# Kernel optimization log

Measured on AMD Instinct MI355X. Metric: run time of the kernel, lower is better.

The kernel has to match this reference:

```python
import jax, jax.numpy as jnp
import numpy as np

B, F_IN, D_IN = 1024, 64, 64
N_CAPS, D_CAPS = 32, 64
ROUTINGS = 3
HEADS = 2
EPS = 1e-7  # K.epsilon()


def setup_inputs() -> dict:
    key = jax.random.key(0)
    ks = jax.random.split(key, 8)
    P = N_CAPS * (N_CAPS - 1) // 2
    return {
        "x": jax.random.normal(ks[0], (B, F_IN, D_IN), jnp.float32),
        "reweight_W": jax.random.normal(ks[1], (D_IN, N_CAPS, D_CAPS), jnp.float32) * 0.05,
        "routing_init": 10.0 * jax.random.truncated_normal(ks[2], -2.0, 2.0, (N_CAPS, F_IN), jnp.float32),
        "kernel_fm": jnp.full((N_CAPS, 1), 0.5, jnp.float32),
        "bias_fm": jnp.zeros((D_CAPS,), jnp.float32),
        "kernel_mf": jnp.ones((P, 1), jnp.float32),
        "bias_mf": jnp.zeros((D_CAPS,), jnp.float32),
        "kernel_highint": jnp.full((N_CAPS, 1), 0.5, jnp.float32),
        "bias_highint": jnp.zeros((D_CAPS * HEADS,), jnp.float32),
        "W_query": jax.random.normal(ks[3], (D_CAPS, D_CAPS * HEADS), jnp.float32) * 0.05,
        "W_key": jax.random.normal(ks[4], (D_CAPS, D_CAPS * HEADS), jnp.float32) * 0.05,
        "W_value": jax.random.normal(ks[5], (D_CAPS, D_CAPS * HEADS), jnp.float32) * 0.05,
        "W_res": jax.random.normal(ks[6], (D_CAPS, D_CAPS * HEADS), jnp.float32) * 0.05,
    }


def _squash(v):
    s = jnp.sum(v * v, axis=-1, keepdims=True) + EPS
    return (jnp.sqrt(s) / (0.5 + s)) * v


def _heads(t):
    # [B,N,H*F] -> [H,B,N,F] (matches tf.stack(tf.split(t, H, axis=2)))
    b, n, _ = t.shape
    return t.reshape(b, n, HEADS, D_CAPS).transpose(2, 0, 1, 3)


def reference(x, reweight_W, routing_init, kernel_fm, bias_fm, kernel_mf, bias_mf,
              kernel_highint, bias_highint, W_query, W_key, W_value, W_res):
    # inputs_hat: [B, N, F, C]
    inputs_hat = jnp.einsum('bfd,dnc->bnfc', x, reweight_W)
    b_logits = jnp.broadcast_to(routing_init[None], (x.shape[0], N_CAPS, F_IN))
    for _ in range(ROUTINGS):
        c = jax.nn.softmax(b_logits, axis=1)            # softmax over capsules
        outputs = _squash(jnp.einsum('bnf,bnfc->bnc', c, inputs_hat))
        b_logits = b_logits + jnp.einsum('bnc,bnfc->bnf', outputs, inputs_hat)
    c = jax.nn.softmax(b_logits, axis=1)
    routing_score = c[..., None]                        # [B,N,F,1]
    attention_output = routing_score * inputs_hat       # [B,N,F,C]

    # FM per-field: square-of-sum minus sum-of-square over input capsules
    sum_f = jnp.sum(attention_output, axis=2)           # [B,N,C]
    field_fm = sum_f ** 2 - jnp.sum(attention_output ** 2, axis=2)
    hi_fm = jnp.sum(field_fm * kernel_fm[None], axis=1) + bias_fm  # [B,C]

    field_wise_vectors = sum_f                          # [B,N,C]

    # pairwise MF interactions (itertools.combinations order == triu indices)
    li, ri = np.triu_indices(N_CAPS, k=1)
    emb_prod = field_wise_vectors[:, li] * field_wise_vectors[:, ri]  # [B,P,C]
    h_mf = jnp.sum(emb_prod * kernel_mf[None], axis=1) + bias_mf      # [B,C]

    # InteractingLayer (multi-head self-attention over fields, use_res=True)
    q = _heads(jnp.einsum('bnd,de->bne', field_wise_vectors, W_query))  # [H,B,N,F]
    k = _heads(jnp.einsum('bnd,de->bne', field_wise_vectors, W_key))
    v = _heads(jnp.einsum('bnd,de->bne', field_wise_vectors, W_value))
    attn = jax.nn.softmax(jnp.einsum('hbnf,hbmf->hbnm', q, k), axis=-1)
    out = jnp.einsum('hbnm,hbmf->hbnf', attn, v)        # [H,B,N,F]
    out = out.transpose(1, 2, 0, 3).reshape(x.shape[0], N_CAPS, HEADS * D_CAPS)
    res = jnp.einsum('bnd,de->bne', field_wise_vectors, W_res)
    fv2 = jax.nn.relu(out + res)                        # [B,N,H*F]
    high_int = jnp.sum(fv2 * kernel_highint[None], axis=1) + bias_highint  # [B,2C]

    return jnp.concatenate([hi_fm, h_mf, high_int], axis=-1), routing_score
```

## Files before the change

kernel.cpp:

```cpp
#include <hip/hip_runtime.h>


#define EPS_SQ 1e-7f

typedef __attribute__((ext_vector_type(8))) short bf16x8;
typedef __attribute__((ext_vector_type(4))) float floatx4;

__device__ __forceinline__ int lidx(int r, int c) {
  return r * 68 + ((((c >> 2) ^ (r >> 2)) & 15) << 2) + (c & 3);
}
__device__ __forceinline__ unsigned short f2bf(float f) {
  unsigned u = __float_as_uint(f);
  u += 0x7FFFu + ((u >> 16) & 1u);
  return (unsigned short)(u >> 16);
}

__global__ __launch_bounds__(256) void k_upd(
    const float* __restrict__ x, const float* __restrict__ rinit,
    const float* __restrict__ ow, float* __restrict__ blog,
    float* __restrict__ xc, float* __restrict__ rs, int iter)
{
  __shared__ __align__(16) float xs[64 * 68];
  __shared__ __align__(16) float owS[32 * 68];
  __shared__ __align__(16) float bS[32 * 68];
  const int b = blockIdx.x, t = threadIdx.x;
  const float* xb = x + b * 4096;

#pragma unroll
  for (int k = 0; k < 4; k++) {
    int lin = t + 256 * k; int f = lin >> 4; int d0 = (lin & 15) << 2;
    *(float4*)&xs[lidx(f, d0)] = *(const float4*)(xb + f * 64 + d0);
  }
  {
    const float* src = (iter <= 1) ? rinit : (blog + b * 2048);
#pragma unroll
    for (int k = 0; k < 2; k++) {
      int lin = t + 256 * k; int n = lin >> 4; int f0 = (lin & 15) << 2;
      *(float4*)&bS[lidx(n, f0)] = *(const float4*)(src + n * 64 + f0);
    }
  }
  if (iter > 0) {
#pragma unroll
    for (int k = 0; k < 2; k++) {
      int lin = t + 256 * k; int n = lin >> 4; int d0 = (lin & 15) << 2;
      *(float4*)&owS[lidx(n, d0)] = *(const float4*)(ow + b * 2048 + n * 64 + d0);
    }
  }
  __syncthreads();

  const int tn = t >> 4, tlo = t & 15;

  if (iter > 0) {
    const int n0 = tn * 2, f0 = tlo * 4;
    float acc[2][4] = {{0, 0, 0, 0}, {0, 0, 0, 0}};
    for (int dq = 0; dq < 64; dq += 4) {
      float o[2][4];
      *(float4*)o[0] = *(const float4*)&owS[lidx(n0, dq)];
      *(float4*)o[1] = *(const float4*)&owS[lidx(n0 + 1, dq)];
#pragma unroll
      for (int i = 0; i < 4; i++) {
        float xr[4];
        *(float4*)xr = *(const float4*)&xs[lidx(f0 + i, dq)];
#pragma unroll
        for (int k = 0; k < 4; k++) {
          acc[0][i] += o[0][k] * xr[k];
          acc[1][i] += o[1][k] * xr[k];
        }
      }
    }
#pragma unroll
    for (int j = 0; j < 2; j++) {
      float tmp[4];
      *(float4*)tmp = *(const float4*)&bS[lidx(n0 + j, f0)];
#pragma unroll
      for (int i = 0; i < 4; i++) tmp[i] += acc[j][i];
      *(float4*)&bS[lidx(n0 + j, f0)] = *(float4*)tmp;
    }
    __syncthreads();
    if (iter < 3) {
#pragma unroll
      for (int k = 0; k < 2; k++) {
        int lin = t + 256 * k; int n = lin >> 4; int f0b = (lin & 15) << 2;
        *(float4*)(blog + b * 2048 + n * 64 + f0b) = *(const float4*)&bS[lidx(n, f0b)];
      }
    }
    __syncthreads();
  }

  {
    const int n = t & 31, fg = t >> 5;
#pragma unroll
    for (int k = 0; k < 8; k++) {
      int f = fg * 8 + k;
      float v = bS[lidx(n, f)];
      float m = v;
      for (int s = 16; s > 0; s >>= 1) m = fmaxf(m, __shfl_xor(m, s, 64));
      float e = __expf(v - m);
      float sum = e;
      for (int s = 16; s > 0; s >>= 1) sum += __shfl_xor(sum, s, 64);
      bS[lidx(n, f)] = e / sum;
    }
  }
  __syncthreads();

  if (iter == 3) {
#pragma unroll
    for (int k = 0; k < 8; k++) {
      int lin = t + 256 * k; int n = lin >> 6, f = lin & 63;
      rs[b * 2048 + n * 64 + f] = bS[lidx(n, f)];
    }
  }
  {
    const int n0 = tn * 2, d0 = tlo * 4;
    float acc[2][4] = {{0, 0, 0, 0}, {0, 0, 0, 0}};
    for (int f = 0; f < 64; f++) {
      float c0v = bS[lidx(n0, f)];
      float c1v = bS[lidx(n0 + 1, f)];
      float xr[4];
      *(float4*)xr = *(const float4*)&xs[lidx(f, d0)];
#pragma unroll
      for (int i = 0; i < 4; i++) {
        acc[0][i] += c0v * xr[i];
        acc[1][i] += c1v * xr[i];
      }
    }
#pragma unroll
    for (int j = 0; j < 2; j++)
      *(float4*)(xc + b * 2048 + (n0 + j) * 64 + d0) = *(float4*)acc[j];
  }
}

__global__ __launch_bounds__(256) void k_sow(
    const float* __restrict__ W, const float* __restrict__ xc,
    float* __restrict__ ow)
{
  __shared__ __align__(16) float Mn[64 * 68];
  __shared__ __align__(16) float xcS[32 * 68];
  __shared__ __align__(16) float sS[32 * 68];
  __shared__ float scaleS[32];
  const int n = blockIdx.x & 31, b0 = (blockIdx.x >> 5) * 32, t = threadIdx.x;

#pragma unroll
  for (int k = 0; k < 4; k++) {
    int lin = t + 256 * k; int d = lin >> 4; int c0 = (lin & 15) << 2;
    *(float4*)&Mn[lidx(d, c0)] = *(const float4*)(W + d * 2048 + n * 64 + c0);
  }
#pragma unroll
  for (int k = 0; k < 2; k++) {
    int lin = t + 256 * k; int bb = lin >> 4; int d0 = (lin & 15) << 2;
    *(float4*)&xcS[lidx(bb, d0)] = *(const float4*)(xc + (b0 + bb) * 2048 + n * 64 + d0);
  }
  __syncthreads();

  const int bb0 = (t >> 4) * 2, c4 = (t & 15) * 4;
  {
    float acc[2][4] = {};
    for (int dq = 0; dq < 64; dq += 4) {
      float xv0[4], xv1[4];
      *(float4*)xv0 = *(const float4*)&xcS[lidx(bb0, dq)];
      *(float4*)xv1 = *(const float4*)&xcS[lidx(bb0 + 1, dq)];
#pragma unroll
      for (int j = 0; j < 4; j++) {
        float mr[4];
        *(float4*)mr = *(const float4*)&Mn[lidx(dq + j, c4)];
#pragma unroll
        for (int c = 0; c < 4; c++) {
          acc[0][c] += xv0[j] * mr[c];
          acc[1][c] += xv1[j] * mr[c];
        }
      }
    }
    *(float4*)&sS[lidx(bb0, c4)] = *(float4*)acc[0];
    *(float4*)&sS[lidx(bb0 + 1, c4)] = *(float4*)acc[1];
  }
  __syncthreads();
  if (t < 32) {
    float ss = EPS_SQ;
    for (int c = 0; c < 64; c++) { float v = sS[lidx(t, c)]; ss += v * v; }
    scaleS[t] = sqrtf(ss) / (0.5f + ss);
  }
  __syncthreads();
  {
    float a2[2][4] = {};
    for (int cq = 0; cq < 64; cq += 4) {
      float sv0[4], sv1[4];
      *(float4*)sv0 = *(const float4*)&sS[lidx(bb0, cq)];
      *(float4*)sv1 = *(const float4*)&sS[lidx(bb0 + 1, cq)];
#pragma unroll
      for (int j = 0; j < 4; j++) {
        float mr[4];
        *(float4*)mr = *(const float4*)&Mn[lidx(c4 + j, cq)];
        float s0 = 0.f, s1 = 0.f;
#pragma unroll
        for (int k = 0; k < 4; k++) { s0 += sv0[k] * mr[k]; s1 += sv1[k] * mr[k]; }
        a2[0][j] += s0; a2[1][j] += s1;
      }
    }
#pragma unroll
    for (int i = 0; i < 2; i++) {
      float sc = scaleS[bb0 + i];
      float outv[4];
#pragma unroll
      for (int j = 0; j < 4; j++) outv[j] = a2[i][j] * sc;
      *(float4*)(ow + (b0 + bb0 + i) * 2048 + n * 64 + c4) = *(float4*)outv;
    }
  }
}

__global__ __launch_bounds__(256) void k_fwv(
    const float* __restrict__ W, const float* __restrict__ xc,
    float* __restrict__ fwv)
{
  __shared__ __align__(16) float Mn[64 * 68];
  __shared__ __align__(16) float xcS[32 * 68];
  const int n = blockIdx.x & 31, b0 = (blockIdx.x >> 5) * 32, t = threadIdx.x;

#pragma unroll
  for (int k = 0; k < 4; k++) {
    int lin = t + 256 * k; int d = lin >> 4; int c0 = (lin & 15) << 2;
    *(float4*)&Mn[lidx(d, c0)] = *(const float4*)(W + d * 2048 + n * 64 + c0);
  }
#pragma unroll
  for (int k = 0; k < 2; k++) {
    int lin = t + 256 * k; int bb = lin >> 4; int d0 = (lin & 15) << 2;
    *(float4*)&xcS[lidx(bb, d0)] = *(const float4*)(xc + (b0 + bb) * 2048 + n * 64 + d0);
  }
  __syncthreads();

  const int bb0 = (t >> 4) * 2, c4 = (t & 15) * 4;
  float acc[2][4] = {};
  for (int dq = 0; dq < 64; dq += 4) {
    float xv0[4], xv1[4];
    *(float4*)xv0 = *(const float4*)&xcS[lidx(bb0, dq)];
    *(float4*)xv1 = *(const float4*)&xcS[lidx(bb0 + 1, dq)];
#pragma unroll
    for (int j = 0; j < 4; j++) {
      float mr[4];
      *(float4*)mr = *(const float4*)&Mn[lidx(dq + j, c4)];
#pragma unroll
      for (int c = 0; c < 4; c++) {
        acc[0][c] += xv0[j] * mr[c];
        acc[1][c] += xv1[j] * mr[c];
      }
    }
  }
  *(float4*)(fwv + (b0 + bb0) * 2048 + n * 64 + c4) = *(float4*)acc[0];
  *(float4*)(fwv + (b0 + bb0 + 1) * 2048 + n * 64 + c4) = *(float4*)acc[1];
}

__global__ __launch_bounds__(256) void k_ih(
    const float* __restrict__ x, const float* __restrict__ W,
    const float* __restrict__ rs, float* __restrict__ ssq)
{
  __shared__ __align__(16) unsigned short xB[4 * 64 * 64];
  __shared__ __align__(16) unsigned short wB[2 * 64 * 64];
  __shared__ float cF2[4 * 2 * 64];
  const int n0 = (blockIdx.x & 15) * 2, g = blockIdx.x >> 4;
  const int b0 = g * 4;
  const int t = threadIdx.x, w = t >> 6, lane = t & 63;

#pragma unroll
  for (int k = 0; k < 16; k++) {
    int ch = t + 256 * k;
    int bb = ch >> 10, rem = ch & 1023;
    int f = rem >> 4, fq = rem & 15;
    int dg = fq >> 1, half = fq & 1;
    float4 v = *(const float4*)(x + ((b0 + bb) * 64 + f) * 64 + fq * 4);
    unsigned int p0 = f2bf(v.x) | ((unsigned)f2bf(v.y) << 16);
    unsigned int p1 = f2bf(v.z) | ((unsigned)f2bf(v.w) << 16);
    *(uint2*)&xB[bb * 4096 + f * 64 + ((dg ^ (f & 7)) << 3) + half * 4] =
        make_uint2(p0, p1);
  }
  {
    int dd = t >> 2, cq = t & 3;
    int dg = dd >> 3, dl = dd & 7;
#pragma unroll
    for (int nn = 0; nn < 2; nn++) {
      const float* wp = W + dd * 2048 + (n0 + nn) * 64 + cq * 16;
      unsigned short* base = wB + nn * 4096;
#pragma unroll
      for (int i4 = 0; i4 < 4; i4++) {
        float4 v = *(const float4*)(wp + i4 * 4);
        float vv[4] = {v.x, v.y, v.z, v.w};
#pragma unroll
        for (int j = 0; j < 4; j++) {
          int c = cq * 16 + i4 * 4 + j;
          base[c * 64 + ((dg ^ (c & 7)) << 3) + dl] = f2bf(vv[j]);
        }
      }
    }
  }
  {
#pragma unroll
    for (int nn = 0; nn < 2; nn++) {
      float v = rs[(b0 + w) * 2048 + (n0 + nn) * 64 + lane];
      cF2[(w * 2 + nn) * 64 + lane] = v * v;
    }
  }
  __syncthreads();

  const int m = lane & 15, q = lane >> 4, ms = m & 7;

  bf16x8 a[4][2];
#pragma unroll
  for (int mi = 0; mi < 4; mi++) {
    const unsigned short* bp = xB + w * 4096 + (mi * 16 + m) * 64;
#pragma unroll
    for (int kk = 0; kk < 2; kk++)
      a[mi][kk] = *(const bf16x8*)&bp[((kk * 4 + q) ^ ms) << 3];
  }

#pragma unroll
  for (int nn = 0; nn < 2; nn++) {
    bf16x8 bf[4][2];
#pragma unroll
    for (int ci = 0; ci < 4; ci++) {
      const unsigned short* bp = wB + nn * 4096 + (ci * 16 + m) * 64;
#pragma unroll
      for (int kk = 0; kk < 2; kk++)
        bf[ci][kk] = *(const bf16x8*)&bp[((kk * 4 + q) ^ ms) << 3];
    }
    float ps[4] = {0.f, 0.f, 0.f, 0.f};
    const float* cf = cF2 + (w * 2 + nn) * 64 + q * 4;
#pragma unroll
    for (int mi = 0; mi < 4; mi++) {
      float cfv[4];
#pragma unroll
      for (int r = 0; r < 4; r++) cfv[r] = cf[mi * 16 + r];
#pragma unroll
      for (int ci = 0; ci < 4; ci++) {
        floatx4 c0 = {0.f, 0.f, 0.f, 0.f};
        c0 = __builtin_amdgcn_mfma_f32_16x16x32_bf16(a[mi][0], bf[ci][0], c0, 0, 0, 0);
        c0 = __builtin_amdgcn_mfma_f32_16x16x32_bf16(a[mi][1], bf[ci][1], c0, 0, 0, 0);
#pragma unroll
        for (int r = 0; r < 4; r++) { float tv = c0[r]; ps[ci] += cfv[r] * tv * tv; }
      }
    }
#pragma unroll
    for (int ci = 0; ci < 4; ci++) {
      ps[ci] += __shfl_xor(ps[ci], 16, 64);
      ps[ci] += __shfl_xor(ps[ci], 32, 64);
    }
    if (q == 0) {
#pragma unroll
      for (int ci = 0; ci < 4; ci++)
        ssq[(b0 + w) * 2048 + (n0 + nn) * 64 + ci * 16 + m] = ps[ci];
    }
  }
}

__global__ __launch_bounds__(256) void k_prep(
    const float* __restrict__ Wq, const float* __restrict__ Wk,
    const float* __restrict__ kmf, float* __restrict__ Ab, float* __restrict__ Kb)
{
  const int t = threadIdx.x;
  if (blockIdx.x < 8) {
    __shared__ __align__(16) float wkS[64 * 68];
    __shared__ __align__(16) float wqS[16 * 68];
    const int h = blockIdx.x & 1, rg = blockIdx.x >> 1;
#pragma unroll
    for (int k = 0; k < 4; k++) {
      int lin = t + 256 * k; int dp = lin >> 4; int e0 = (lin & 15) << 2;
      *(float4*)&wkS[lidx(dp, e0)] = *(const float4*)(Wk + dp * 128 + h * 64 + e0);
    }
    {
      int dl = t >> 4, e0 = (t & 15) << 2;
      *(float4*)&wqS[lidx(dl, e0)] = *(const float4*)(Wq + (rg * 16 + dl) * 128 + h * 64 + e0);
    }
    __syncthreads();
    const int dl = t >> 4, dp0 = (t & 15) << 2;
    float acc[4] = {};
    for (int e = 0; e < 64; e += 4) {
      float q4[4];
      *(float4*)q4 = *(const float4*)&wqS[lidx(dl, e)];
#pragma unroll
      for (int c = 0; c < 4; c++) {
        float mr[4];
        *(float4*)mr = *(const float4*)&wkS[lidx(dp0 + c, e)];
        acc[c] += q4[0] * mr[0] + q4[1] * mr[1] + q4[2] * mr[2] + q4[3] * mr[3];
      }
    }
    *(float4*)(Ab + h * 4096 + (rg * 16 + dl) * 64 + dp0) = *(float4*)acc;
  } else {
    __shared__ float Ks[1024];
    *(float4*)&Ks[t * 4] = make_float4(0.f, 0.f, 0.f, 0.f);
    __syncthreads();
    if (t < 248) {
#pragma unroll
      for (int j = 0; j < 2; j++) {
        int p = t * 2 + j;
        if (p < 496) {
          int l = 0, rem = p;
          while (rem >= 31 - l) { rem -= 31 - l; ++l; }
          int r = l + 1 + rem;
          float v = kmf[p];
          Ks[l * 32 + r] = v;
          Ks[r * 32 + l] = v;
        }
      }
    }
    __syncthreads();
    *(float4*)&Kb[t * 4] = *(const float4*)&Ks[t * 4];
  }
}

__global__ __launch_bounds__(256) void k_attn(
    const float* __restrict__ fwv, const float* __restrict__ ssq,
    const float* __restrict__ Ab, const float* __restrict__ Kb,
    const float* __restrict__ Wv, const float* __restrict__ Wr,
    const float* __restrict__ kfm, const float* __restrict__ bfm,
    const float* __restrict__ bmf, const float* __restrict__ khi,
    const float* __restrict__ bhi, float* __restrict__ out0)
{
  __shared__ __align__(16) float smem[8640];
  float* fwS  = smem;
  float* pS   = smem + 2176;
  float* bufA = smem + 4288;
  float* tS   = smem + 6464;
  float* vS   = smem + 4288;
  float* redH = smem + 2176;
  float* Kf   = smem + 4288;
  float* red1 = smem + 5312;

  const int b = blockIdx.x, t = threadIdx.x;
  const int tn = t >> 4, te = t & 15;
  const int n0 = tn * 2, e0 = te * 8, d0 = te * 4;

#pragma unroll
  for (int k = 0; k < 2; k++) {
    int lin = t + 256 * k; int nn = lin >> 4; int c0 = (lin & 15) << 2;
    *(float4*)&fwS[lidx(nn, c0)] = *(const float4*)(fwv + b * 2048 + nn * 64 + c0);
  }
  __syncthreads();

  for (int h = 0; h < 2; h++) {
    float tacc[2][4] = {};
    for (int half = 0; half < 2; half++) {
#pragma unroll
      for (int k = 0; k < 2; k++) {
        int lin = t + 256 * k; int d = lin >> 4; int c0 = (lin & 15) << 2;
        *(float4*)&bufA[lidx(d, c0)] =
            *(const float4*)(Ab + h * 4096 + (half * 32 + d) * 64 + c0);
      }
      __syncthreads();
      for (int dq = 0; dq < 32; dq += 4) {
        float fw0[4], fw1[4];
        *(float4*)fw0 = *(const float4*)&fwS[lidx(n0, half * 32 + dq)];
        *(float4*)fw1 = *(const float4*)&fwS[lidx(n0 + 1, half * 32 + dq)];
#pragma unroll
        for (int j = 0; j < 4; j++) {
          float mr[4];
          *(float4*)mr = *(const float4*)&bufA[lidx(dq + j, d0)];
#pragma unroll
          for (int c = 0; c < 4; c++) {
            tacc[0][c] += fw0[j] * mr[c];
            tacc[1][c] += fw1[j] * mr[c];
          }
        }
      }
      __syncthreads();
    }
    *(float4*)&tS[lidx(n0, d0)] = *(float4*)tacc[0];
    *(float4*)&tS[lidx(n0 + 1, d0)] = *(float4*)tacc[1];
    __syncthreads();
    {
      const int m0 = te * 2;
      float s00 = 0.f, s01 = 0.f, s10 = 0.f, s11 = 0.f;
      for (int kk = 0; kk < 16; kk++) {
        float ta0[4], ta1[4], f0[4], f1[4];
        *(float4*)ta0 = *(const float4*)&tS[lidx(n0, kk * 4)];
        *(float4*)ta1 = *(const float4*)&tS[lidx(n0 + 1, kk * 4)];
        *(float4*)f0 = *(const float4*)&fwS[lidx(m0, kk * 4)];
        *(float4*)f1 = *(const float4*)&fwS[lidx(m0 + 1, kk * 4)];
#pragma unroll
        for (int j = 0; j < 4; j++) {
          s00 += ta0[j] * f0[j]; s01 += ta0[j] * f1[j];
          s10 += ta1[j] * f0[j]; s11 += ta1[j] * f1[j];
        }
      }
      pS[(h * 32 + n0) * 33 + m0] = s00;
      pS[(h * 32 + n0) * 33 + m0 + 1] = s01;
      pS[(h * 32 + n0 + 1) * 33 + m0] = s10;
      pS[(h * 32 + n0 + 1) * 33 + m0 + 1] = s11;
    }
    __syncthreads();
  }

  if (t < 64) {
    const int base = t * 33;
    float mx = -1e30f;
    for (int m = 0; m < 32; m++) mx = fmaxf(mx, pS[base + m]);
    float sum = 0.f;
    for (int m = 0; m < 32; m++) { float e = __expf(pS[base + m] - mx); pS[base + m] = e; sum += e; }
    float inv = 1.0f / sum;
    for (int m = 0; m < 32; m++) pS[base + m] *= inv;
  }
  __syncthreads();

  {
    float acc[2][8] = {};
    for (int dq = 0; dq < 64; dq += 4) {
      float fw0[4], fw1[4];
      *(float4*)fw0 = *(const float4*)&fwS[lidx(n0, dq)];
      *(float4*)fw1 = *(const float4*)&fwS[lidx(n0 + 1, dq)];
#pragma unroll
      for (int jj = 0; jj < 4; jj++) {
        float w8[8];
        *(float4*)&w8[0] = *(const float4*)(Wv + (dq + jj) * 128 + e0);
        *(float4*)&w8[4] = *(const float4*)(Wv + (dq + jj) * 128 + e0 + 4);
#pragma unroll
        for (int j = 0; j < 8; j++) {
          acc[0][j] += fw0[jj] * w8[j];
          acc[1][j] += fw1[jj] * w8[j];
        }
      }
    }
    *(float4*)&vS[n0 * 132 + e0] = *(float4*)&acc[0][0];
    *(float4*)&vS[n0 * 132 + e0 + 4] = *(float4*)&acc[0][4];
    *(float4*)&vS[(n0 + 1) * 132 + e0] = *(float4*)&acc[1][0];
    *(float4*)&vS[(n0 + 1) * 132 + e0 + 4] = *(float4*)&acc[1][4];
  }
  __syncthreads();

  {
    const int h2 = te >> 3;
    float pacc[2][8] = {};
    for (int m = 0; m < 32; m++) {
      float p0 = pS[(h2 * 32 + n0) * 33 + m];
      float p1 = pS[(h2 * 32 + n0 + 1) * 33 + m];
      float vr[8];
      *(float4*)&vr[0] = *(const float4*)&vS[m * 132 + e0];
      *(float4*)&vr[4] = *(const float4*)&vS[m * 132 + e0 + 4];
#pragma unroll
      for (int j = 0; j < 8; j++) {
        pacc[0][j] += p0 * vr[j];
        pacc[1][j] += p1 * vr[j];
      }
    }
    for (int dq = 0; dq < 64; dq += 4) {
      float fw0[4], fw1[4];
      *(float4*)fw0 = *(const float4*)&fwS[lidx(n0, dq)];
      *(float4*)fw1 = *(const float4*)&fwS[lidx(n0 + 1, dq)];
#pragma unroll
      for (int jj = 0; jj < 4; jj++) {
        float w8[8];
        *(float4*)&w8[0] = *(const float4*)(Wr + (dq + jj) * 128 + e0);
        *(float4*)&w8[4] = *(const float4*)(Wr + (dq + jj) * 128 + e0 + 4);
#pragma unroll
        for (int j = 0; j < 8; j++) {
          pacc[0][j] += fw0[jj] * w8[j];
          pacc[1][j] += fw1[jj] * w8[j];
        }
      }
    }
    __syncthreads();
    {
      float kh0 = khi[n0], kh1 = khi[n0 + 1];
      float ph[8];
#pragma unroll
      for (int j = 0; j < 8; j++)
        ph[j] = kh0 * fmaxf(pacc[0][j], 0.f) + kh1 * fmaxf(pacc[1][j], 0.f);
      *(float4*)&redH[tn * 132 + e0] = *(float4*)&ph[0];
      *(float4*)&redH[tn * 132 + e0 + 4] = *(float4*)&ph[4];
    }
  }
  *(float4*)&Kf[t * 4] = *(const float4*)(Kb + t * 4);
  __syncthreads();

  if (t < 128) {
    float s = 0.f;
#pragma unroll
    for (int k = 0; k < 16; k++) s += redH[k * 132 + t];
    out0[b * 256 + 128 + t] = s + bhi[t];
  }
  {
    const int c = t & 63, nq = t >> 6;
    float p = 0.f;
#pragma unroll
    for (int k = 0; k < 8; k++) {
      int nn = nq * 8 + k;
      float fv = fwS[lidx(nn, c)];
      float sv = ssq[b * 2048 + nn * 64 + c];
      p += (fv * fv - sv) * kfm[nn];
    }
    red1[nq * 68 + c] = p;
    float inner[8] = {};
    for (int r = 0; r < 32; r++) {
      float fr = fwS[lidx(r, c)];
#pragma unroll
      for (int l8 = 0; l8 < 8; l8++)
        inner[l8] += Kf[(nq * 8 + l8) * 32 + r] * fr;
    }
    float hmf = 0.f;
#pragma unroll
    for (int l8 = 0; l8 < 8; l8++)
      hmf += fwS[lidx(nq * 8 + l8, c)] * inner[l8];
    red1[(4 + nq) * 68 + c] = hmf;
  }
  __syncthreads();
  if (t < 64) {
    out0[b * 256 + t] = red1[t] + red1[68 + t] + red1[136 + t] + red1[204 + t] + bfm[t];
    float h2 = red1[272 + t] + red1[340 + t] + red1[408 + t] + red1[476 + t];
    out0[b * 256 + 64 + t] = 0.5f * h2 + bmf[t];
  }
}

extern "C" void kernel_launch(void* const* d_in, const int* in_sizes, int n_in,
                              void* d_out, int out_size, void* d_ws, size_t ws_size,
                              hipStream_t stream) {
  (void)in_sizes; (void)n_in; (void)out_size; (void)ws_size;
  const float* x     = (const float*)d_in[0];
  const float* W     = (const float*)d_in[1];
  const float* rinit = (const float*)d_in[2];
  const float* kfm   = (const float*)d_in[3];
  const float* bfm   = (const float*)d_in[4];
  const float* kmf   = (const float*)d_in[5];
  const float* bmf   = (const float*)d_in[6];
  const float* khi   = (const float*)d_in[7];
  const float* bhi   = (const float*)d_in[8];
  const float* Wq    = (const float*)d_in[9];
  const float* Wk    = (const float*)d_in[10];
  const float* Wv    = (const float*)d_in[11];
  const float* Wr    = (const float*)d_in[12];

  float* out0 = (float*)d_out;
  float* rs   = out0 + 1024 * 256;

  float* ws   = (float*)d_ws;
  float* xc   = ws;
  float* ow   = ws + 2097152;
  float* blog = ws + 2 * 2097152;
  float* fwv  = ow;
  float* ssq  = blog;
  float* Abuf = xc;
  float* Kbuf = xc + 8192;

  k_upd<<<1024, 256, 0, stream>>>(x, rinit, ow, blog, xc, rs, 0);
  for (int it = 1; it <= 3; it++) {
    k_sow<<<1024, 256, 0, stream>>>(W, xc, ow);
    k_upd<<<1024, 256, 0, stream>>>(x, rinit, ow, blog, xc, rs, it);
  }
  k_fwv<<<1024, 256, 0, stream>>>(W, xc, fwv);
  k_prep<<<9, 256, 0, stream>>>(Wq, Wk, kmf, Abuf, Kbuf);
  k_ih<<<4096, 256, 0, stream>>>(x, W, rs, ssq);
  k_attn<<<1024, 256, 0, stream>>>(fwv, ssq, Abuf, Kbuf, Wv, Wr,
                                   kfm, bfm, bmf, khi, bhi, out0);
}
```

Measured before the change: 293.0 us.

## Precompute per-capsule Gram matrix for routing and batch capsules in ih kernel

Routing now precomputes Q_n = W_n W_n^T once per capsule. Each iteration then does a single matvec y = Q xc, and takes the squash norm as xc·y through a wave shuffle. This replaces the two chained matmuls and the shared-memory norm pass in the old sow kernel. The ih kernel now covers eight capsules per block, so each x tile is converted to bf16 once and reused, cutting the grid from 4096 to 1024 blocks; the squared routing scores are stored as bf16, which loses some precision. The attention softmax is split across four lanes per row with float4 accesses, and rows are padded to 36 floats. Q is staged in the routing-score output buffer before the final scores overwrite it.

```diff
diff --git a/kernel.cpp b/kernel.cpp
--- a/kernel.cpp
+++ b/kernel.cpp
@@ -130,21 +130,53 @@
   }
 }
 
-__global__ __launch_bounds__(256) void k_sow(
-    const float* __restrict__ W, const float* __restrict__ xc,
-    float* __restrict__ ow)
+__global__ __launch_bounds__(256) void k_prepq(
+    const float* __restrict__ W, float* __restrict__ Qb)
 {
   __shared__ __align__(16) float Mn[64 * 68];
-  __shared__ __align__(16) float xcS[32 * 68];
-  __shared__ __align__(16) float sS[32 * 68];
-  __shared__ float scaleS[32];
-  const int n = blockIdx.x & 31, b0 = (blockIdx.x >> 5) * 32, t = threadIdx.x;
-
+  const int n = blockIdx.x, t = threadIdx.x;
 #pragma unroll
   for (int k = 0; k < 4; k++) {
     int lin = t + 256 * k; int d = lin >> 4; int c0 = (lin & 15) << 2;
     *(float4*)&Mn[lidx(d, c0)] = *(const float4*)(W + d * 2048 + n * 64 + c0);
   }
+  __syncthreads();
+  const int d1 = (t >> 4) * 4, d2 = (t & 15) * 4;
+  float acc[4][4] = {};
+  for (int cq = 0; cq < 64; cq += 4) {
+    float m1[4][4], m2[4][4];
+#pragma unroll
+    for (int i = 0; i < 4; i++) *(float4*)m1[i] = *(const float4*)&Mn[lidx(d1 + i, cq)];
+#pragma unroll
+    for (int j = 0; j < 4; j++) *(float4*)m2[j] = *(const float4*)&Mn[lidx(d2 + j, cq)];
+#pragma unroll
+    for (int i = 0; i < 4; i++)
+#pragma unroll
+      for (int j = 0; j < 4; j++) {
+        float s = 0.f;
+#pragma unroll
+        for (int k = 0; k < 4; k++) s += m1[i][k] * m2[j][k];
+        acc[i][j] += s;
+      }
+  }
+#pragma unroll
+  for (int i = 0; i < 4; i++)
+    *(float4*)(Qb + n * 4096 + (d1 + i) * 64 + d2) = *(float4*)acc[i];
+}
+
+__global__ __launch_bounds__(256) void k_sowq(
+    const float* __restrict__ Qb, const float* __restrict__ xc,
+    float* __restrict__ ow)
+{
+  __shared__ __align__(16) float Qs[64 * 68];
+  __shared__ __align__(16) float xcS[32 * 68];
+  const int n = blockIdx.x & 31, b0 = (blockIdx.x >> 5) * 32, t = threadIdx.x;
+
+#pragma unroll
+  for (int k = 0; k < 4; k++) {
+    int lin = t + 256 * k; int d1 = lin >> 4; int d2 = (lin & 15) << 2;
+    *(float4*)&Qs[lidx(d1, d2)] = *(const float4*)(Qb + n * 4096 + d1 * 64 + d2);
+  }
 #pragma unroll
   for (int k = 0; k < 2; k++) {
     int lin = t + 256 * k; int bb = lin >> 4; int d0 = (lin & 15) << 2;
@@ -152,59 +184,42 @@
   }
   __syncthreads();
 
-  const int bb0 = (t >> 4) * 2, c4 = (t & 15) * 4;
-  {
-    float acc[2][4] = {};
-    for (int dq = 0; dq < 64; dq += 4) {
-      float xv0[4], xv1[4];
-      *(float4*)xv0 = *(const float4*)&xcS[lidx(bb0, dq)];
-      *(float4*)xv1 = *(const float4*)&xcS[lidx(bb0 + 1, dq)];
-#pragma unroll
-      for (int j = 0; j < 4; j++) {
-        float mr[4];
-        *(float4*)mr = *(const float4*)&Mn[lidx(dq + j, c4)];
-#pragma unroll
-        for (int c = 0; c < 4; c++) {
-          acc[0][c] += xv0[j] * mr[c];
-          acc[1][c] += xv1[j] * mr[c];
-        }
-      }
-    }
-    *(float4*)&sS[lidx(bb0, c4)] = *(float4*)acc[0];
-    *(float4*)&sS[lidx(bb0 + 1, c4)] = *(float4*)acc[1];
-  }
-  __syncthreads();
-  if (t < 32) {
-    float ss = EPS_SQ;
-    for (int c = 0; c < 64; c++) { float v = sS[lidx(t, c)]; ss += v * v; }
-    scaleS[t] = sqrtf(ss) / (0.5f + ss);
-  }
-  __syncthreads();
-  {
-    float a2[2][4] = {};
-    for (int cq = 0; cq < 64; cq += 4) {
-      float sv0[4], sv1[4];
-      *(float4*)sv0 = *(const float4*)&sS[lidx(bb0, cq)];
-      *(float4*)sv1 = *(const float4*)&sS[lidx(bb0 + 1, cq)];
-#pragma unroll
-      for (int j = 0; j < 4; j++) {
-        float mr[4];
-        *(float4*)mr = *(const float4*)&Mn[lidx(c4 + j, cq)];
-        float s0 = 0.f, s1 = 0.f;
-#pragma unroll
-        for (int k = 0; k < 4; k++) { s0 += sv0[k] * mr[k]; s1 += sv1[k] * mr[k]; }
-        a2[0][j] += s0; a2[1][j] += s1;
-      }
-    }
-#pragma unroll
-    for (int i = 0; i < 2; i++) {
-      float sc = scaleS[bb0 + i];
-      float outv[4];
-#pragma unroll
-      for (int j = 0; j < 4; j++) outv[j] = a2[i][j] * sc;
-      *(float4*)(ow + (b0 + bb0 + i) * 2048 + n * 64 + c4) = *(float4*)outv;
-    }
-  }
+  const int bb0 = (t >> 4) * 2, d4 = (t & 15) * 4;
+  float y0[4] = {}, y1[4] = {};
+  for (int dq = 0; dq < 64; dq += 4) {
+    float x0[4], x1[4];
+    *(float4*)x0 = *(const float4*)&xcS[lidx(bb0, dq)];
+    *(float4*)x1 = *(const float4*)&xcS[lidx(bb0 + 1, dq)];
+#pragma unroll
+    for (int j = 0; j < 4; j++) {
+      float qr[4];
+      *(float4*)qr = *(const float4*)&Qs[lidx(dq + j, d4)];
+#pragma unroll
+      for (int c = 0; c < 4; c++) {
+        y0[c] += x0[j] * qr[c];
+        y1[c] += x1[j] * qr[c];
+      }
+    }
+  }
+  float xa[4], xb2[4];
+  *(float4*)xa = *(const float4*)&xcS[lidx(bb0, d4)];
+  *(float4*)xb2 = *(const float4*)&xcS[lidx(bb0 + 1, d4)];
+  float s0 = 0.f, s1 = 0.f;
+#pragma unroll
+  for (int c = 0; c < 4; c++) { s0 += y0[c] * xa[c]; s1 += y1[c] * xb2[c]; }
+#pragma unroll
+  for (int sh = 1; sh <= 8; sh <<= 1) {
+    s0 += __shfl_xor(s0, sh, 64);
+    s1 += __shfl_xor(s1, sh, 64);
+  }
+  s0 += EPS_SQ; s1 += EPS_SQ;
+  const float sc0 = sqrtf(s0) / (0.5f + s0);
+  const float sc1 = sqrtf(s1) / (0.5f + s1);
+  float o0[4], o1[4];
+#pragma unroll
+  for (int c = 0; c < 4; c++) { o0[c] = y0[c] * sc0; o1[c] = y1[c] * sc1; }
+  *(float4*)(ow + (b0 + bb0) * 2048 + n * 64 + d4) = *(float4*)o0;
+  *(float4*)(ow + (b0 + bb0 + 1) * 2048 + n * 64 + d4) = *(float4*)o1;
 }
 
 __global__ __launch_bounds__(256) void k_fwv(
@@ -254,9 +269,8 @@
 {
   __shared__ __align__(16) unsigned short xB[4 * 64 * 64];
   __shared__ __align__(16) unsigned short wB[2 * 64 * 64];
-  __shared__ float cF2[4 * 2 * 64];
-  const int n0 = (blockIdx.x & 15) * 2, g = blockIdx.x >> 4;
-  const int b0 = g * 4;
+  __shared__ unsigned short cF2[4 * 8 * 64];
+  const int n_oct = (blockIdx.x & 3) << 3, b0 = (blockIdx.x >> 2) * 4;
   const int t = threadIdx.x, w = t >> 6, lane = t & 63;
 
 #pragma unroll
@@ -266,41 +280,19 @@
     int f = rem >> 4, fq = rem & 15;
     int dg = fq >> 1, half = fq & 1;
     float4 v = *(const float4*)(x + ((b0 + bb) * 64 + f) * 64 + fq * 4);
-    unsigned int p0 = f2bf(v.x) | ((unsigned)f2bf(v.y) << 16);
-    unsigned int p1 = f2bf(v.z) | ((unsigned)f2bf(v.w) << 16);
+    unsigned p0 = f2bf(v.x) | ((unsigned)f2bf(v.y) << 16);
+    unsigned p1 = f2bf(v.z) | ((unsigned)f2bf(v.w) << 16);
     *(uint2*)&xB[bb * 4096 + f * 64 + ((dg ^ (f & 7)) << 3) + half * 4] =
         make_uint2(p0, p1);
   }
-  {
-    int dd = t >> 2, cq = t & 3;
-    int dg = dd >> 3, dl = dd & 7;
-#pragma unroll
-    for (int nn = 0; nn < 2; nn++) {
-      const float* wp = W + dd * 2048 + (n0 + nn) * 64 + cq * 16;
-      unsigned short* base = wB + nn * 4096;
-#pragma unroll
-      for (int i4 = 0; i4 < 4; i4++) {
-        float4 v = *(const float4*)(wp + i4 * 4);
-        float vv[4] = {v.x, v.y, v.z, v.w};
-#pragma unroll
-        for (int j = 0; j < 4; j++) {
-          int c = cq * 16 + i4 * 4 + j;
-          base[c * 64 + ((dg ^ (c & 7)) << 3) + dl] = f2bf(vv[j]);
-        }
-      }
-    }
-  }
-  {
-#pragma unroll
-    for (int nn = 0; nn < 2; nn++) {
-      float v = rs[(b0 + w) * 2048 + (n0 + nn) * 64 + lane];
-      cF2[(w * 2 + nn) * 64 + lane] = v * v;
-    }
+#pragma unroll
+  for (int nn = 0; nn < 8; nn++) {
+    float v = rs[(b0 + w) * 2048 + (n_oct + nn) * 64 + lane];
+    cF2[(w * 8 + nn) * 64 + lane] = f2bf(v * v);
   }
   __syncthreads();
 
   const int m = lane & 15, q = lane >> 4, ms = m & 7;
-
   bf16x8 a[4][2];
 #pragma unroll
   for (int mi = 0; mi < 4; mi++) {
@@ -310,41 +302,66 @@
       a[mi][kk] = *(const bf16x8*)&bp[((kk * 4 + q) ^ ms) << 3];
   }
 
-#pragma unroll
-  for (int nn = 0; nn < 2; nn++) {
-    bf16x8 bf[4][2];
-#pragma unroll
-    for (int ci = 0; ci < 4; ci++) {
-      const unsigned short* bp = wB + nn * 4096 + (ci * 16 + m) * 64;
-#pragma unroll
-      for (int kk = 0; kk < 2; kk++)
-        bf[ci][kk] = *(const bf16x8*)&bp[((kk * 4 + q) ^ ms) << 3];
-    }
-    float ps[4] = {0.f, 0.f, 0.f, 0.f};
-    const float* cf = cF2 + (w * 2 + nn) * 64 + q * 4;
-#pragma unroll
-    for (int mi = 0; mi < 4; mi++) {
-      float cfv[4];
-#pragma unroll
-      for (int r = 0; r < 4; r++) cfv[r] = cf[mi * 16 + r];
+  for (int np = 0; np < 4; np++) {
+    const int n0 = n_oct + np * 2;
+    __syncthreads();
+    {
+      int dd = t >> 2, cq = t & 3;
+      int dg = dd >> 3, dl = dd & 7;
+#pragma unroll
+      for (int nn = 0; nn < 2; nn++) {
+        const float* wp = W + dd * 2048 + (n0 + nn) * 64 + cq * 16;
+        unsigned short* base = wB + nn * 4096;
+#pragma unroll
+        for (int i4 = 0; i4 < 4; i4++) {
+          float4 v = *(const float4*)(wp + i4 * 4);
+          float vv[4] = {v.x, v.y, v.z, v.w};
+#pragma unroll
+          for (int j = 0; j < 4; j++) {
+            int c = cq * 16 + i4 * 4 + j;
+            base[c * 64 + ((dg ^ (c & 7)) << 3) + dl] = f2bf(vv[j]);
+          }
+        }
+      }
+    }
+    __syncthreads();
+#pragma unroll
+    for (int nn = 0; nn < 2; nn++) {
+      bf16x8 bf[4][2];
 #pragma unroll
       for (int ci = 0; ci < 4; ci++) {
-        floatx4 c0 = {0.f, 0.f, 0.f, 0.f};
-        c0 = __builtin_amdgcn_mfma_f32_16x16x32_bf16(a[mi][0], bf[ci][0], c0, 0, 0, 0);
-        c0 = __builtin_amdgcn_mfma_f32_16x16x32_bf16(a[mi][1], bf[ci][1], c0, 0, 0, 0);
-#pragma unroll
-        for (int r = 0; r < 4; r++) { float tv = c0[r]; ps[ci] += cfv[r] * tv * tv; }
-      }
-    }
-#pragma unroll
-    for (int ci = 0; ci < 4; ci++) {
-      ps[ci] += __shfl_xor(ps[ci], 16, 64);
-      ps[ci] += __shfl_xor(ps[ci], 32, 64);
-    }
-    if (q == 0) {
-#pragma unroll
-      for (int ci = 0; ci < 4; ci++)
-        ssq[(b0 + w) * 2048 + (n0 + nn) * 64 + ci * 16 + m] = ps[ci];
+        const unsigned short* bp = wB + nn * 4096 + (ci * 16 + m) * 64;
+#pragma unroll
+        for (int kk = 0; kk < 2; kk++)
+          bf[ci][kk] = *(const bf16x8*)&bp[((kk * 4 + q) ^ ms) << 3];
+      }
+      float ps[4] = {0.f, 0.f, 0.f, 0.f};
+      const unsigned short* cf = cF2 + (w * 8 + np * 2 + nn) * 64 + q * 4;
+#pragma unroll
+      for (int mi = 0; mi < 4; mi++) {
+        float cfv[4];
+#pragma unroll
+        for (int r = 0; r < 4; r++)
+          cfv[r] = __uint_as_float((unsigned)cf[mi * 16 + r] << 16);
+#pragma unroll
+        for (int ci = 0; ci < 4; ci++) {
+          floatx4 c0 = {0.f, 0.f, 0.f, 0.f};
+          c0 = __builtin_amdgcn_mfma_f32_16x16x32_bf16(a[mi][0], bf[ci][0], c0, 0, 0, 0);
+          c0 = __builtin_amdgcn_mfma_f32_16x16x32_bf16(a[mi][1], bf[ci][1], c0, 0, 0, 0);
+#pragma unroll
+          for (int r = 0; r < 4; r++) { float tv = c0[r]; ps[ci] += cfv[r] * tv * tv; }
+        }
+      }
+#pragma unroll
+      for (int ci = 0; ci < 4; ci++) {
+        ps[ci] += __shfl_xor(ps[ci], 16, 64);
+        ps[ci] += __shfl_xor(ps[ci], 32, 64);
+      }
+      if (q == 0) {
+#pragma unroll
+        for (int ci = 0; ci < 4; ci++)
+          ssq[(b0 + w) * 2048 + (n0 + nn) * 64 + ci * 16 + m] = ps[ci];
+      }
     }
   }
 }
@@ -412,15 +429,15 @@
     const float* __restrict__ bmf, const float* __restrict__ khi,
     const float* __restrict__ bhi, float* __restrict__ out0)
 {
-  __shared__ __align__(16) float smem[8640];
+  __shared__ __align__(16) float smem[8832];
   float* fwS  = smem;
   float* pS   = smem + 2176;
-  float* bufA = smem + 4288;
-  float* tS   = smem + 6464;
-  float* vS   = smem + 4288;
+  float* bufA = smem + 4480;
+  float* tS   = smem + 6656;
+  float* vS   = smem + 4480;
   float* redH = smem + 2176;
-  float* Kf   = smem + 4288;
-  float* red1 = smem + 5312;
+  float* Kf   = smem + 4480;
+  float* red1 = smem + 5504;
 
   const int b = blockIdx.x, t = threadIdx.x;
   const int tn = t >> 4, te = t & 15;
@@ -478,22 +495,36 @@
           s10 += ta1[j] * f0[j]; s11 += ta1[j] * f1[j];
         }
       }
-      pS[(h * 32 + n0) * 33 + m0] = s00;
-      pS[(h * 32 + n0) * 33 + m0 + 1] = s01;
-      pS[(h * 32 + n0 + 1) * 33 + m0] = s10;
-      pS[(h * 32 + n0 + 1) * 33 + m0 + 1] = s11;
-    }
-    __syncthreads();
-  }
-
-  if (t < 64) {
-    const int base = t * 33;
-    float mx = -1e30f;
-    for (int m = 0; m < 32; m++) mx = fmaxf(mx, pS[base + m]);
+      pS[(h * 32 + n0) * 36 + m0] = s00;
+      pS[(h * 32 + n0) * 36 + m0 + 1] = s01;
+      pS[(h * 32 + n0 + 1) * 36 + m0] = s10;
+      pS[(h * 32 + n0 + 1) * 36 + m0 + 1] = s11;
+    }
+    __syncthreads();
+  }
+
+  {
+    const int r = t >> 2, sub = t & 3;
+    const int base = r * 36 + sub * 8;
+    float v0[4], v1[4];
+    *(float4*)v0 = *(const float4*)&pS[base];
+    *(float4*)v1 = *(const float4*)&pS[base + 4];
+    float mx = fmaxf(fmaxf(fmaxf(v0[0], v0[1]), fmaxf(v0[2], v0[3])),
+                     fmaxf(fmaxf(v1[0], v1[1]), fmaxf(v1[2], v1[3])));
+    mx = fmaxf(mx, __shfl_xor(mx, 1, 64));
+    mx = fmaxf(mx, __shfl_xor(mx, 2, 64));
     float sum = 0.f;
-    for (int m = 0; m < 32; m++) { float e = __expf(pS[base + m] - mx); pS[base + m] = e; sum += e; }
-    float inv = 1.0f / sum;
-    for (int m = 0; m < 32; m++) pS[base + m] *= inv;
+#pragma unroll
+    for (int j = 0; j < 4; j++) { v0[j] = __expf(v0[j] - mx); sum += v0[j]; }
+#pragma unroll
+    for (int j = 0; j < 4; j++) { v1[j] = __expf(v1[j] - mx); sum += v1[j]; }
+    sum += __shfl_xor(sum, 1, 64);
+    sum += __shfl_xor(sum, 2, 64);
+    const float inv = 1.0f / sum;
+#pragma unroll
+    for (int j = 0; j < 4; j++) { v0[j] *= inv; v1[j] *= inv; }
+    *(float4*)&pS[base] = *(float4*)v0;
+    *(float4*)&pS[base + 4] = *(float4*)v1;
   }
   __syncthreads();
 
@@ -526,8 +557,8 @@
     const int h2 = te >> 3;
     float pacc[2][8] = {};
     for (int m = 0; m < 32; m++) {
-      float p0 = pS[(h2 * 32 + n0) * 33 + m];
-      float p1 = pS[(h2 * 32 + n0 + 1) * 33 + m];
+      float p0 = pS[(h2 * 32 + n0) * 36 + m];
+      float p1 = pS[(h2 * 32 + n0 + 1) * 36 + m];
       float vr[8];
       *(float4*)&vr[0] = *(const float4*)&vS[m * 132 + e0];
       *(float4*)&vr[4] = *(const float4*)&vS[m * 132 + e0 + 4];
@@ -625,6 +656,7 @@
 
   float* out0 = (float*)d_out;
   float* rs   = out0 + 1024 * 256;
+  float* Qbuf = rs;
 
   float* ws   = (float*)d_ws;
   float* xc   = ws;
@@ -635,14 +667,15 @@
   float* Abuf = xc;
   float* Kbuf = xc + 8192;
 
+  k_prepq<<<32, 256, 0, stream>>>(W, Qbuf);
   k_upd<<<1024, 256, 0, stream>>>(x, rinit, ow, blog, xc, rs, 0);
   for (int it = 1; it <= 3; it++) {
-    k_sow<<<1024, 256, 0, stream>>>(W, xc, ow);
+    k_sowq<<<1024, 256, 0, stream>>>(Qbuf, xc, ow);
     k_upd<<<1024, 256, 0, stream>>>(x, rinit, ow, blog, xc, rs, it);
   }
   k_fwv<<<1024, 256, 0, stream>>>(W, xc, fwv);
   k_prep<<<9, 256, 0, stream>>>(Wq, Wk, kmf, Abuf, Kbuf);
-  k_ih<<<4096, 256, 0, stream>>>(x, W, rs, ssq);
+  k_ih<<<1024, 256, 0, stream>>>(x, W, rs, ssq);
   k_attn<<<1024, 256, 0, stream>>>(fwv, ssq, Abuf, Kbuf, Wv, Wr,
                                    kfm, bfm, bmf, khi, bhi, out0);
 }
```

Measured after the change: 280.5 us. 4.3% less time.
